# Kernel tuning notes

Hardware: AMD Instinct MI355X
Metric: run time of the kernel (lower is better)

The kernel has to match this reference:

```python
import jax, jax.numpy as jnp
import numpy as np

D_MODEL = 1024
N_HEADS = 16
HEAD_DIM = 64
INNER = N_HEADS * HEAD_DIM  # 1024


def setup_inputs() -> dict:
    key = jax.random.key(0)
    ks = jax.random.split(key, 5)
    x = jax.random.normal(ks[0], (4, 2048, D_MODEL), dtype=jnp.float32)
    ln_w = jnp.ones((D_MODEL,), dtype=jnp.float32)
    ln_b = jnp.zeros((D_MODEL,), dtype=jnp.float32)
    w_qkv = jax.random.normal(ks[1], (D_MODEL, 3 * INNER), dtype=jnp.float32) * (D_MODEL ** -0.5)
    w_out = jax.random.normal(ks[2], (INNER, D_MODEL), dtype=jnp.float32) * (INNER ** -0.5)
    return {"x": x, "ln_w": ln_w, "ln_b": ln_b, "w_qkv": w_qkv, "w_out": w_out}


def reference(x, ln_w, ln_b, w_qkv, w_out):
    eps = 1e-5
    scale = HEAD_DIM ** -0.5
    # LayerNorm over last dim
    mu = jnp.mean(x, axis=-1, keepdims=True)
    var = jnp.mean(jnp.square(x - mu), axis=-1, keepdims=True)
    h = (x - mu) * jax.lax.rsqrt(var + eps) * ln_w + ln_b
    # QKV projection: [b, n, 3*inner]
    qkv = h @ w_qkv
    q, k, v = jnp.split(qkv, 3, axis=-1)
    b, n, _ = q.shape
    def heads(t):
        return t.reshape(b, n, N_HEADS, HEAD_DIM).transpose(0, 2, 1, 3)  # b h n d
    q, k, v = heads(q), heads(k), heads(v)
    dots = jnp.einsum('bhnd,bhmd->bhnm', q, k) * scale  # [b,h,n,n]
    attn = jax.nn.softmax(dots, axis=-1)
    out = jnp.einsum('bhnm,bhmd->bhnd', attn, v)
    out = out.transpose(0, 2, 1, 3).reshape(b, n, INNER)
    return out @ w_out
```

## Files before the change

kernel.cpp:

```cpp
#include <hip/hip_runtime.h>
#include <hip/hip_bf16.h>

typedef __bf16 bf16x8 __attribute__((ext_vector_type(8)));
typedef float f32x4 __attribute__((ext_vector_type(4)));
typedef short s16x4 __attribute__((ext_vector_type(4)));

#define D_MODEL 1024
#define N_SEQ   2048
#define N_BATCH 4
#define N_HEADS 16
#define HEAD_DIM 64
#define M_ROWS  (N_BATCH * N_SEQ)
#define N_QKV   (3 * D_MODEL)
#define CS2     0.18033688f

__device__ __forceinline__ void async_copy16(const void* g, void* s) {
    __builtin_amdgcn_global_load_lds(
        (const __attribute__((address_space(1))) unsigned*)g,
        (__attribute__((address_space(3))) unsigned*)s, 16, 0, 0);
}

__global__ __launch_bounds__(256) void ln_kernel(
    const float* __restrict__ x, const float* __restrict__ w,
    const float* __restrict__ b, __hip_bfloat16* __restrict__ h)
{
    __shared__ float red[8];
    long row = blockIdx.x;
    int tid = threadIdx.x;
    float4 xv = *(const float4*)&x[row * D_MODEL + tid * 4];
    float s = xv.x + xv.y + xv.z + xv.w;
    #pragma unroll
    for (int o = 32; o; o >>= 1) s += __shfl_down(s, o);
    if ((tid & 63) == 0) red[tid >> 6] = s;
    __syncthreads();
    float mu = (red[0] + red[1] + red[2] + red[3]) * (1.f / 1024.f);
    float d0 = xv.x - mu, d1 = xv.y - mu, d2 = xv.z - mu, d3 = xv.w - mu;
    float vs = d0 * d0 + d1 * d1 + d2 * d2 + d3 * d3;
    #pragma unroll
    for (int o = 32; o; o >>= 1) vs += __shfl_down(vs, o);
    if ((tid & 63) == 0) red[4 + (tid >> 6)] = vs;
    __syncthreads();
    float var = (red[4] + red[5] + red[6] + red[7]) * (1.f / 1024.f);
    float inv = rsqrtf(var + 1e-5f);
    float4 wv = *(const float4*)&w[tid * 4];
    float4 bv = *(const float4*)&b[tid * 4];
    union { ushort4 u; __hip_bfloat16 h[4]; } o4;
    o4.h[0] = __float2bfloat16(d0 * inv * wv.x + bv.x);
    o4.h[1] = __float2bfloat16(d1 * inv * wv.y + bv.y);
    o4.h[2] = __float2bfloat16(d2 * inv * wv.z + bv.z);
    o4.h[3] = __float2bfloat16(d3 * inv * wv.w + bv.w);
    *(ushort4*)&h[row * D_MODEL + tid * 4] = o4.u;
}

__global__ __launch_bounds__(256) void transpose_cast(
    const float* __restrict__ src, __hip_bfloat16* __restrict__ dst, int R, int C)
{
    __shared__ float tile[32][33];
    int tx = threadIdx.x, ty = threadIdx.y;
    int c0 = blockIdx.x * 32, r0 = blockIdx.y * 32;
    #pragma unroll
    for (int j = 0; j < 32; j += 8)
        tile[ty + j][tx] = src[(long)(r0 + ty + j) * C + c0 + tx];
    __syncthreads();
    #pragma unroll
    for (int j = 0; j < 32; j += 8)
        dst[(long)(c0 + ty + j) * R + r0 + tx] = __float2bfloat16(tile[tx][ty + j]);
}

__global__ __launch_bounds__(256) void gemm_bt(
    const __hip_bfloat16* __restrict__ A, const __hip_bfloat16* __restrict__ Bt,
    int M, int Nn, int K, int mode,
    __hip_bfloat16* __restrict__ qb, __hip_bfloat16* __restrict__ kb,
    __hip_bfloat16* __restrict__ vbt, float* __restrict__ outp)
{
    __shared__ __hip_bfloat16 smem[128 * 136];
    __hip_bfloat16* As = smem;
    __hip_bfloat16* Bs = smem + 4096;
    int tid = threadIdx.x;
    int wave = tid >> 6, lane = tid & 63, quad = lane >> 4, l15 = lane & 15;
    int wm = (wave >> 1) * 64, wn = (wave & 1) * 64;
    long bm = blockIdx.y, bn = blockIdx.x;
    bool swapop = (mode == 1) && (bn < 16);

    f32x4 acc[4][4] = {};

    for (int k0 = 0; k0 < K; k0 += 32) {
        __syncthreads();
        #pragma unroll
        for (int s = 0; s < 2; ++s) {
            int seg = tid + s * 256;
            int row = seg >> 2, c8 = (seg & 3) * 8;
            async_copy16(&A[(bm * 128 + row) * K + k0 + c8], &As[seg * 8]);
            async_copy16(&Bt[(bn * 128 + row) * K + k0 + c8], &Bs[seg * 8]);
        }
        __syncthreads();
        bf16x8 af[4], bfr[4];
        #pragma unroll
        for (int t = 0; t < 4; ++t) {
            af[t]  = *(const bf16x8*)&As[(wm + t * 16 + l15) * 32 + quad * 8];
            bfr[t] = *(const bf16x8*)&Bs[(wn + t * 16 + l15) * 32 + quad * 8];
        }
        if (swapop) {
            #pragma unroll
            for (int tm = 0; tm < 4; ++tm)
                #pragma unroll
                for (int tn = 0; tn < 4; ++tn)
                    acc[tm][tn] = __builtin_amdgcn_mfma_f32_16x16x32_bf16(
                        bfr[tn], af[tm], acc[tm][tn], 0, 0, 0);
        } else {
            #pragma unroll
            for (int tm = 0; tm < 4; ++tm)
                #pragma unroll
                for (int tn = 0; tn < 4; ++tn)
                    acc[tm][tn] = __builtin_amdgcn_mfma_f32_16x16x32_bf16(
                        af[tm], bfr[tn], acc[tm][tn], 0, 0, 0);
        }
    }

    if (mode == 0) {
        #pragma unroll
        for (int tm = 0; tm < 4; ++tm)
            #pragma unroll
            for (int tn = 0; tn < 4; ++tn)
                #pragma unroll
                for (int r = 0; r < 4; ++r) {
                    long row = bm * 128 + wm + tm * 16 + quad * 4 + r;
                    long col = bn * 128 + wn + tn * 16 + l15;
                    outp[row * Nn + col] = acc[tm][tn][r];
                }
        return;
    }

    int which = (int)(bn >> 3);
    __syncthreads();
    if (which < 2) {
        float esc = (which == 0) ? CS2 : 1.0f;
        #pragma unroll
        for (int tm = 0; tm < 4; ++tm)
            #pragma unroll
            for (int tn = 0; tn < 4; ++tn) {
                union { ushort4 u; __hip_bfloat16 h[4]; } pk;
                #pragma unroll
                for (int r = 0; r < 4; ++r)
                    pk.h[r] = __float2bfloat16(acc[tm][tn][r] * esc);
                *(ushort4*)&smem[(wm + tm * 16 + l15) * 136 + wn + tn * 16 + quad * 4] = pk.u;
            }
        __syncthreads();
        __hip_bfloat16* ptr = (which == 0) ? qb : kb;
        #pragma unroll
        for (int it = 0; it < 8; ++it) {
            int idx = it * 256 + tid;
            int lr = idx >> 4, lc = (idx & 15) * 8;
            uint4 vv = *(const uint4*)&smem[lr * 136 + lc];
            long row = bm * 128 + lr;
            long bb = row >> 11, n = row & 2047;
            int cg = (int)bn * 128 + lc - which * 1024;
            int head = cg >> 6, d = cg & 63;
            *(uint4*)&ptr[(((bb * 16 + head) * 2048) + n) * 64 + d] = vv;
        }
    } else {
        #pragma unroll
        for (int tm = 0; tm < 4; ++tm)
            #pragma unroll
            for (int tn = 0; tn < 4; ++tn) {
                union { ushort4 u; __hip_bfloat16 h[4]; } pk;
                #pragma unroll
                for (int r = 0; r < 4; ++r)
                    pk.h[r] = __float2bfloat16(acc[tm][tn][r]);
                *(ushort4*)&smem[(wn + tn * 16 + l15) * 136 + wm + tm * 16 + quad * 4] = pk.u;
            }
        __syncthreads();
        #pragma unroll
        for (int it = 0; it < 8; ++it) {
            int idx = it * 256 + tid;
            int lr = idx >> 4, lc = (idx & 15) * 8;
            uint4 vv = *(const uint4*)&smem[lr * 136 + lc];
            int cg = (int)bn * 128 + lr - 2048;
            int head = cg >> 6, d = cg & 63;
            long nrow = bm * 128 + lc;
            long bb = nrow >> 11, n = nrow & 2047;
            *(uint4*)&vbt[((bb * 16 + head) * 64 + d) * 2048 + n] = vv;
        }
    }
}

__global__ __launch_bounds__(256) void attn_kernel(
    const __hip_bfloat16* __restrict__ q, const __hip_bfloat16* __restrict__ k,
    const __hip_bfloat16* __restrict__ vt, __hip_bfloat16* __restrict__ ao)
{
    __shared__ __hip_bfloat16 Ks[64][68];
    __shared__ __hip_bfloat16 Vs[64][68];
    int tid = threadIdx.x;
    int wave = tid >> 6, lane = tid & 63, quad = lane >> 4, l15 = lane & 15;
    int bh = blockIdx.y;
    int q0 = blockIdx.x * 128;
    const long base = (long)bh * N_SEQ * HEAD_DIM;

    bf16x8 qf[2][2];
    #pragma unroll
    for (int qs = 0; qs < 2; ++qs)
        #pragma unroll
        for (int hh = 0; hh < 2; ++hh)
            qf[qs][hh] = *(const bf16x8*)&q[base
                + (long)(q0 + wave * 32 + qs * 16 + l15) * HEAD_DIM
                + hh * 32 + quad * 8];

    f32x4 Oacc[2][4] = {};
    float l_run[2] = { 0.f, 0.f };
    union PFrag { s16x4 v; __hip_bfloat16 h[4]; };
    PFrag pfr[2][4];

    int sr[2], sc[2];
    #pragma unroll
    for (int s = 0; s < 2; ++s) {
        int seg = tid + s * 256;
        sr[s] = seg >> 3; sc[s] = (seg & 7) * 8;
    }

    uint4 kpre[2], vpre[2];
    #pragma unroll
    for (int s = 0; s < 2; ++s) {
        kpre[s] = *(const uint4*)&k[base + (long)sr[s] * HEAD_DIM + sc[s]];
        vpre[s] = *(const uint4*)&vt[base + (long)sr[s] * N_SEQ + sc[s]];
    }

    for (int kt = 0; kt < N_SEQ / 64; ++kt) {
        __syncthreads();
        #pragma unroll
        for (int s = 0; s < 2; ++s) {
            *(uint4*)&Ks[sr[s]][sc[s]] = kpre[s];
            *(uint4*)&Vs[sr[s]][sc[s]] = vpre[s];
        }
        __syncthreads();
        if (kt + 1 < N_SEQ / 64) {
            int key1 = (kt + 1) * 64;
            #pragma unroll
            for (int s = 0; s < 2; ++s) {
                kpre[s] = *(const uint4*)&k[base + (long)(key1 + sr[s]) * HEAD_DIM + sc[s]];
                vpre[s] = *(const uint4*)&vt[base + (long)sr[s] * N_SEQ + key1 + sc[s]];
            }
        }

        bf16x8 kf[4][2];
        #pragma unroll
        for (int tk = 0; tk < 4; ++tk)
            #pragma unroll
            for (int hh = 0; hh < 2; ++hh)
                kf[tk][hh] = *(const bf16x8*)&Ks[tk * 16 + l15][hh * 32 + quad * 8];

        #pragma unroll
        for (int qs = 0; qs < 2; ++qs) {
            #pragma unroll
            for (int tk = 0; tk < 4; ++tk) {
                f32x4 a = {};
                a = __builtin_amdgcn_mfma_f32_16x16x32_bf16(kf[tk][0], qf[qs][0], a, 0, 0, 0);
                a = __builtin_amdgcn_mfma_f32_16x16x32_bf16(kf[tk][1], qf[qs][1], a, 0, 0, 0);
                float rs = 0.f;
                #pragma unroll
                for (int r = 0; r < 4; ++r) {
                    float pv = exp2f(a[r]);
                    pfr[qs][tk].h[r] = __float2bfloat16(pv);
                    rs += pv;
                }
                l_run[qs] += rs;
            }
        }

        #pragma unroll
        for (int dt = 0; dt < 4; ++dt) {
            s16x4 vf[4];
            #pragma unroll
            for (int tk = 0; tk < 4; ++tk)
                vf[tk] = *(const s16x4*)&Vs[dt * 16 + l15][tk * 16 + quad * 4];
            #pragma unroll
            for (int qs = 0; qs < 2; ++qs)
                #pragma unroll
                for (int tk = 0; tk < 4; ++tk)
                    Oacc[qs][dt] = __builtin_amdgcn_mfma_f32_16x16x16bf16_1k(
                        vf[tk], pfr[qs][tk].v, Oacc[qs][dt], 0, 0, 0);
        }
    }

    int b = bh >> 4, h = bh & 15;
    #pragma unroll
    for (int qs = 0; qs < 2; ++qs) {
        float ltot = l_run[qs];
        ltot += __shfl_xor(ltot, 16);
        ltot += __shfl_xor(ltot, 32);
        float linv = 1.f / ltot;
        int n = q0 + wave * 32 + qs * 16 + l15;
        #pragma unroll
        for (int dt = 0; dt < 4; ++dt) {
            union { ushort4 u; __hip_bfloat16 h[4]; } pk;
            #pragma unroll
            for (int r = 0; r < 4; ++r)
                pk.h[r] = __float2bfloat16(Oacc[qs][dt][r] * linv);
            *(ushort4*)&ao[((long)(b * N_SEQ + n)) * D_MODEL
                           + h * HEAD_DIM + dt * 16 + quad * 4] = pk.u;
        }
    }
}

extern "C" void kernel_launch(void* const* d_in, const int* in_sizes, int n_in,
                              void* d_out, int out_size, void* d_ws, size_t ws_size,
                              hipStream_t stream)
{
    const float* x     = (const float*)d_in[0];
    const float* ln_w  = (const float*)d_in[1];
    const float* ln_b  = (const float*)d_in[2];
    const float* w_qkv = (const float*)d_in[3];
    const float* w_out = (const float*)d_in[4];
    float* out = (float*)d_out;

    char* ws = (char*)d_ws;
    __hip_bfloat16* h_bf   = (__hip_bfloat16*)(ws);
    __hip_bfloat16* wqkv_t = (__hip_bfloat16*)(ws + 16777216);
    __hip_bfloat16* wout_t = (__hip_bfloat16*)(ws + 23068672);
    __hip_bfloat16* qb     = (__hip_bfloat16*)(ws + 25165824);
    __hip_bfloat16* kb     = (__hip_bfloat16*)(ws + 41943040);
    __hip_bfloat16* vbt    = (__hip_bfloat16*)(ws + 58720256);
    __hip_bfloat16* ao     = (__hip_bfloat16*)(ws + 75497472);

    ln_kernel<<<M_ROWS, 256, 0, stream>>>(x, ln_w, ln_b, h_bf);
    transpose_cast<<<dim3(N_QKV / 32, D_MODEL / 32), dim3(32, 8), 0, stream>>>(
        w_qkv, wqkv_t, D_MODEL, N_QKV);
    transpose_cast<<<dim3(D_MODEL / 32, D_MODEL / 32), dim3(32, 8), 0, stream>>>(
        w_out, wout_t, D_MODEL, D_MODEL);
    gemm_bt<<<dim3(N_QKV / 128, M_ROWS / 128), 256, 0, stream>>>(
        h_bf, wqkv_t, M_ROWS, N_QKV, D_MODEL, 1, qb, kb, vbt, nullptr);
    attn_kernel<<<dim3(N_SEQ / 128, N_BATCH * N_HEADS), 256, 0, stream>>>(qb, kb, vbt, ao);
    gemm_bt<<<dim3(D_MODEL / 128, M_ROWS / 128), 256, 0, stream>>>(
        ao, wout_t, M_ROWS, D_MODEL, D_MODEL, 0, nullptr, nullptr, nullptr, out);
}
```

Measured before the change: 480.0 us.

## Double-buffer K/V tiles in LDS and swap PV MFMA operand order

The attention kernel now keeps two LDS buffers for K and V and prefetches two tiles ahead. The next tile is written to the alternate buffer while the current one is consumed, which removes one of the two barriers per key tile. The operands of the PV MFMA are swapped, so the accumulator layout is transposed, and the epilogue changes to scalar bf16 stores with per-row normalisers fetched by shuffle. The cost is double the LDS footprint and narrower, less coalesced output stores.

```diff
diff --git a/kernel.cpp b/kernel.cpp
--- a/kernel.cpp
+++ b/kernel.cpp
@@ -188,13 +188,14 @@
     const __hip_bfloat16* __restrict__ q, const __hip_bfloat16* __restrict__ k,
     const __hip_bfloat16* __restrict__ vt, __hip_bfloat16* __restrict__ ao)
 {
-    __shared__ __hip_bfloat16 Ks[64][68];
-    __shared__ __hip_bfloat16 Vs[64][68];
+    __shared__ __hip_bfloat16 Ks[2][64][68];
+    __shared__ __hip_bfloat16 Vs[2][64][68];
     int tid = threadIdx.x;
     int wave = tid >> 6, lane = tid & 63, quad = lane >> 4, l15 = lane & 15;
     int bh = blockIdx.y;
     int q0 = blockIdx.x * 128;
     const long base = (long)bh * N_SEQ * HEAD_DIM;
+    const int NT = N_SEQ / 64;
 
     bf16x8 qf[2][2];
     #pragma unroll
@@ -223,21 +224,33 @@
         kpre[s] = *(const uint4*)&k[base + (long)sr[s] * HEAD_DIM + sc[s]];
         vpre[s] = *(const uint4*)&vt[base + (long)sr[s] * N_SEQ + sc[s]];
     }
-
-    for (int kt = 0; kt < N_SEQ / 64; ++kt) {
-        __syncthreads();
-        #pragma unroll
-        for (int s = 0; s < 2; ++s) {
-            *(uint4*)&Ks[sr[s]][sc[s]] = kpre[s];
-            *(uint4*)&Vs[sr[s]][sc[s]] = vpre[s];
-        }
-        __syncthreads();
-        if (kt + 1 < N_SEQ / 64) {
-            int key1 = (kt + 1) * 64;
+    #pragma unroll
+    for (int s = 0; s < 2; ++s) {
+        *(uint4*)&Ks[0][sr[s]][sc[s]] = kpre[s];
+        *(uint4*)&Vs[0][sr[s]][sc[s]] = vpre[s];
+    }
+    #pragma unroll
+    for (int s = 0; s < 2; ++s) {
+        kpre[s] = *(const uint4*)&k[base + (long)(64 + sr[s]) * HEAD_DIM + sc[s]];
+        vpre[s] = *(const uint4*)&vt[base + (long)sr[s] * N_SEQ + 64 + sc[s]];
+    }
+    __syncthreads();
+
+    for (int kt = 0; kt < NT; ++kt) {
+        int cur = kt & 1, nxt = cur ^ 1;
+        if (kt + 1 < NT) {
             #pragma unroll
             for (int s = 0; s < 2; ++s) {
-                kpre[s] = *(const uint4*)&k[base + (long)(key1 + sr[s]) * HEAD_DIM + sc[s]];
-                vpre[s] = *(const uint4*)&vt[base + (long)sr[s] * N_SEQ + key1 + sc[s]];
+                *(uint4*)&Ks[nxt][sr[s]][sc[s]] = kpre[s];
+                *(uint4*)&Vs[nxt][sr[s]][sc[s]] = vpre[s];
+            }
+        }
+        if (kt + 2 < NT) {
+            int key2 = (kt + 2) * 64;
+            #pragma unroll
+            for (int s = 0; s < 2; ++s) {
+                kpre[s] = *(const uint4*)&k[base + (long)(key2 + sr[s]) * HEAD_DIM + sc[s]];
+                vpre[s] = *(const uint4*)&vt[base + (long)sr[s] * N_SEQ + key2 + sc[s]];
             }
         }
 
@@ -246,7 +259,7 @@
         for (int tk = 0; tk < 4; ++tk)
             #pragma unroll
             for (int hh = 0; hh < 2; ++hh)
-                kf[tk][hh] = *(const bf16x8*)&Ks[tk * 16 + l15][hh * 32 + quad * 8];
+                kf[tk][hh] = *(const bf16x8*)&Ks[cur][tk * 16 + l15][hh * 32 + quad * 8];
 
         #pragma unroll
         for (int qs = 0; qs < 2; ++qs) {
@@ -271,14 +284,15 @@
             s16x4 vf[4];
             #pragma unroll
             for (int tk = 0; tk < 4; ++tk)
-                vf[tk] = *(const s16x4*)&Vs[dt * 16 + l15][tk * 16 + quad * 4];
+                vf[tk] = *(const s16x4*)&Vs[cur][dt * 16 + l15][tk * 16 + quad * 4];
             #pragma unroll
             for (int qs = 0; qs < 2; ++qs)
                 #pragma unroll
                 for (int tk = 0; tk < 4; ++tk)
                     Oacc[qs][dt] = __builtin_amdgcn_mfma_f32_16x16x16bf16_1k(
-                        vf[tk], pfr[qs][tk].v, Oacc[qs][dt], 0, 0, 0);
-        }
+                        pfr[qs][tk].v, vf[tk], Oacc[qs][dt], 0, 0, 0);
+        }
+        __syncthreads();
     }
 
     int b = bh >> 4, h = bh & 15;
@@ -287,17 +301,18 @@
         float ltot = l_run[qs];
         ltot += __shfl_xor(ltot, 16);
         ltot += __shfl_xor(ltot, 32);
-        float linv = 1.f / ltot;
-        int n = q0 + wave * 32 + qs * 16 + l15;
-        #pragma unroll
-        for (int dt = 0; dt < 4; ++dt) {
-            union { ushort4 u; __hip_bfloat16 h[4]; } pk;
-            #pragma unroll
-            for (int r = 0; r < 4; ++r)
-                pk.h[r] = __float2bfloat16(Oacc[qs][dt][r] * linv);
-            *(ushort4*)&ao[((long)(b * N_SEQ + n)) * D_MODEL
-                           + h * HEAD_DIM + dt * 16 + quad * 4] = pk.u;
-        }
+        float linv[4];
+        #pragma unroll
+        for (int r = 0; r < 4; ++r)
+            linv[r] = 1.f / __shfl(ltot, quad * 4 + r);
+        #pragma unroll
+        for (int dt = 0; dt < 4; ++dt)
+            #pragma unroll
+            for (int r = 0; r < 4; ++r) {
+                int n = q0 + wave * 32 + qs * 16 + quad * 4 + r;
+                ao[((long)(b * N_SEQ + n)) * D_MODEL + h * HEAD_DIM + dt * 16 + l15] =
+                    __float2bfloat16(Oacc[qs][dt][r] * linv[r]);
+            }
     }
 }
 
```

Result: faster. 393.5 us (-18.0%).

## Load K/V fragments directly from global memory, dropping LDS staging and barriers

Applied to the files above, without the earlier changes.

The attention kernel no longer stages K and V tiles through shared memory with two block barriers per key tile. Each wave reads its MFMA fragments straight from global memory and relies on cache reuse across the four waves. The PV MFMA operand order is swapped, so the output accumulator layout is transposed and the epilogue now writes scalar bf16 values with per-row normalisers gathered by shuffle. This removes synchronisation and LDS traffic, but it loses the software prefetch, repeats global loads per wave, and makes the output stores narrower and less coalesced.

```diff
diff --git a/kernel.cpp b/kernel.cpp
--- a/kernel.cpp
+++ b/kernel.cpp
@@ -188,13 +188,13 @@
     const __hip_bfloat16* __restrict__ q, const __hip_bfloat16* __restrict__ k,
     const __hip_bfloat16* __restrict__ vt, __hip_bfloat16* __restrict__ ao)
 {
-    __shared__ __hip_bfloat16 Ks[64][68];
-    __shared__ __hip_bfloat16 Vs[64][68];
     int tid = threadIdx.x;
     int wave = tid >> 6, lane = tid & 63, quad = lane >> 4, l15 = lane & 15;
     int bh = blockIdx.y;
     int q0 = blockIdx.x * 128;
     const long base = (long)bh * N_SEQ * HEAD_DIM;
+    const __hip_bfloat16* kp = k + base;
+    const __hip_bfloat16* vp = vt + base;
 
     bf16x8 qf[2][2];
     #pragma unroll
@@ -210,43 +210,24 @@
     union PFrag { s16x4 v; __hip_bfloat16 h[4]; };
     PFrag pfr[2][4];
 
-    int sr[2], sc[2];
-    #pragma unroll
-    for (int s = 0; s < 2; ++s) {
-        int seg = tid + s * 256;
-        sr[s] = seg >> 3; sc[s] = (seg & 7) * 8;
-    }
-
-    uint4 kpre[2], vpre[2];
-    #pragma unroll
-    for (int s = 0; s < 2; ++s) {
-        kpre[s] = *(const uint4*)&k[base + (long)sr[s] * HEAD_DIM + sc[s]];
-        vpre[s] = *(const uint4*)&vt[base + (long)sr[s] * N_SEQ + sc[s]];
-    }
-
     for (int kt = 0; kt < N_SEQ / 64; ++kt) {
-        __syncthreads();
-        #pragma unroll
-        for (int s = 0; s < 2; ++s) {
-            *(uint4*)&Ks[sr[s]][sc[s]] = kpre[s];
-            *(uint4*)&Vs[sr[s]][sc[s]] = vpre[s];
-        }
-        __syncthreads();
-        if (kt + 1 < N_SEQ / 64) {
-            int key1 = (kt + 1) * 64;
-            #pragma unroll
-            for (int s = 0; s < 2; ++s) {
-                kpre[s] = *(const uint4*)&k[base + (long)(key1 + sr[s]) * HEAD_DIM + sc[s]];
-                vpre[s] = *(const uint4*)&vt[base + (long)sr[s] * N_SEQ + key1 + sc[s]];
-            }
-        }
+        int key0 = kt * 64;
+
+        s16x4 vf[4][4];
+        #pragma unroll
+        for (int dt = 0; dt < 4; ++dt)
+            #pragma unroll
+            for (int tk = 0; tk < 4; ++tk)
+                vf[dt][tk] = *(const s16x4*)&vp[(long)(dt * 16 + l15) * N_SEQ
+                                                + key0 + tk * 16 + quad * 4];
 
         bf16x8 kf[4][2];
         #pragma unroll
         for (int tk = 0; tk < 4; ++tk)
             #pragma unroll
             for (int hh = 0; hh < 2; ++hh)
-                kf[tk][hh] = *(const bf16x8*)&Ks[tk * 16 + l15][hh * 32 + quad * 8];
+                kf[tk][hh] = *(const bf16x8*)&kp[(long)(key0 + tk * 16 + l15) * HEAD_DIM
+                                                 + hh * 32 + quad * 8];
 
         #pragma unroll
         for (int qs = 0; qs < 2; ++qs) {
@@ -267,18 +248,13 @@
         }
 
         #pragma unroll
-        for (int dt = 0; dt < 4; ++dt) {
-            s16x4 vf[4];
-            #pragma unroll
-            for (int tk = 0; tk < 4; ++tk)
-                vf[tk] = *(const s16x4*)&Vs[dt * 16 + l15][tk * 16 + quad * 4];
+        for (int dt = 0; dt < 4; ++dt)
             #pragma unroll
             for (int qs = 0; qs < 2; ++qs)
                 #pragma unroll
                 for (int tk = 0; tk < 4; ++tk)
                     Oacc[qs][dt] = __builtin_amdgcn_mfma_f32_16x16x16bf16_1k(
-                        vf[tk], pfr[qs][tk].v, Oacc[qs][dt], 0, 0, 0);
-        }
+                        pfr[qs][tk].v, vf[dt][tk], Oacc[qs][dt], 0, 0, 0);
     }
 
     int b = bh >> 4, h = bh & 15;
@@ -287,17 +263,18 @@
         float ltot = l_run[qs];
         ltot += __shfl_xor(ltot, 16);
         ltot += __shfl_xor(ltot, 32);
-        float linv = 1.f / ltot;
-        int n = q0 + wave * 32 + qs * 16 + l15;
-        #pragma unroll
-        for (int dt = 0; dt < 4; ++dt) {
-            union { ushort4 u; __hip_bfloat16 h[4]; } pk;
-            #pragma unroll
-            for (int r = 0; r < 4; ++r)
-                pk.h[r] = __float2bfloat16(Oacc[qs][dt][r] * linv);
-            *(ushort4*)&ao[((long)(b * N_SEQ + n)) * D_MODEL
-                           + h * HEAD_DIM + dt * 16 + quad * 4] = pk.u;
-        }
+        float linv[4];
+        #pragma unroll
+        for (int r = 0; r < 4; ++r)
+            linv[r] = 1.f / __shfl(ltot, quad * 4 + r);
+        #pragma unroll
+        for (int dt = 0; dt < 4; ++dt)
+            #pragma unroll
+            for (int r = 0; r < 4; ++r) {
+                int n = q0 + wave * 32 + qs * 16 + quad * 4 + r;
+                ao[((long)(b * N_SEQ + n)) * D_MODEL + h * HEAD_DIM + dt * 16 + l15] =
+                    __float2bfloat16(Oacc[qs][dt][r] * linv[r]);
+            }
     }
 }
 
```

New measurement: 653.3 us. +36.1%, slower.
